# Performance work log

Hardware: AMD Instinct MI355X
Metric: run time of the kernel (lower is better)

Reference implementation:

```python
import jax, jax.numpy as jnp
import numpy as np

B, NV, NH = 256, 512, 256


def setup_inputs() -> dict:
    key = jax.random.key(0)
    k1, k2, k3, k4, k5 = jax.random.split(key, 5)
    return {
        "wt": jax.random.normal(k1, (B, NH, NV), dtype=jnp.float32),
        "varh_diag": jax.random.uniform(k2, (B, NH), dtype=jnp.float32),
        "sig2": jax.random.uniform(k3, (B,), dtype=jnp.float32),
        "b": jax.random.normal(k4, (B, NV), dtype=jnp.float32),
        "muh": jax.random.normal(k5, (B, NH), dtype=jnp.float32),
    }


def reference(wt, varh_diag, sig2, b, muh):
    # wt: [B, nh, nv], varh_diag: [B, nh], sig2: [B], b: [B, nv], muh: [B, nh]
    nv = wt.shape[2]
    w = jnp.transpose(wt, (0, 2, 1))                      # [B, nv, nh]
    # diag(varh_diag) @ wt == broadcasted row scaling (avoids materializing diag)
    varvh = varh_diag[:, :, None] * wt                    # [B, nh, nv]
    # varv = w @ varh @ wt + sig2 * I
    varv = jnp.einsum('bvh,bhu->bvu', w, varvh)           # [B, nv, nv]
    varv = varv + sig2[:, None, None] * jnp.eye(nv, dtype=wt.dtype)
    # muv = b + w @ muh
    muv = b + jnp.einsum('bvh,bh->bv', w, muh)            # [B, nv]
    mu = jnp.concatenate([muv, muh], axis=1)              # [B, nv+nh]
    # block covariance: [[varv, varvh^T], [varvh, diag(varh_diag)]]
    varh = jax.vmap(jnp.diag)(varh_diag)                  # [B, nh, nh]
    varvht = jnp.transpose(varvh, (0, 2, 1))              # [B, nv, nh]
    top = jnp.concatenate([varv, varvht], axis=2)         # [B, nv, nv+nh]
    bot = jnp.concatenate([varvh, varh], axis=2)          # [B, nh, nv+nh]
    var = jnp.concatenate([top, bot], axis=1)             # [B, nv+nh, nv+nh]
    return mu, var
```

## Files before the change

kernel.cpp:

```cpp
#include <hip/hip_runtime.h>
#include <hip/hip_bf16.h>

#define B_  256
#define NH  256
#define NV  512
#define NT  768
#define TPB 9

typedef __bf16 bf16x8 __attribute__((ext_vector_type(8)));
typedef float  f32x4  __attribute__((ext_vector_type(4)));

__device__ __forceinline__ __bf16 f2bf(float f) { return static_cast<__bf16>(f); }

__global__ __launch_bounds__(512) void fused(const float* __restrict__ wt,
                                             const float* __restrict__ varh,
                                             const float* __restrict__ sig2,
                                             const float* __restrict__ bvec,
                                             const float* __restrict__ muh,
                                             float* __restrict__ out) {
    __shared__ __align__(16) char smem[76 * 1024];

    const int bid  = blockIdx.x;
    const int q    = bid >> 3;
    const int b    = (bid & 7) * 32 + q / TPB;
    const int tile = q % TPB;
    const int t    = threadIdx.x;

    const float* wtb  = wt + (size_t)b * NH * NV;
    float* mu   = out + (size_t)b * NT;
    float* varb = out + (size_t)B_ * NT + (size_t)b * NT * NT;

    if (tile < 3) {
        const int  mt   = (tile == 1);
        const int  nt   = (tile != 0);
        const bool diag = (tile < 2);

        bf16x8 (*As)[256] = (bf16x8(*)[256])(smem);
        bf16x8 (*Bs)[256] = (bf16x8(*)[256])(smem + 32 * 1024);
        float*  varh_s    = (float*)(smem + 64 * 1024);
        float*  muh_s     = (float*)(smem + 65 * 1024);
        float (*red)[256] = (float(*)[256])(smem + 66 * 1024);

        const int m0 = mt * 256, n0 = nt * 256;
        const int lane = t & 63, wid = t >> 6;
        const int wm = wid >> 2, wn = wid & 3;
        const int mc = t & 63;
        const int kb = t >> 6;

        if (t < NH) { varh_s[t] = varh[b * NH + t]; muh_s[t] = muh[b * NH + t]; }

        f32x4 acc[8][4] = {};
        float acc_mu[4] = {0.f, 0.f, 0.f, 0.f};
        __syncthreads();

        for (int st = 0; st < 4; ++st) {
            const int k0 = st * 64;
            f32x4 av[8], bv[8];
            const float* baseA = wtb + (size_t)(k0 + kb * 8) * NV + m0 + 4 * mc;
#pragma unroll
            for (int j = 0; j < 8; ++j)
                av[j] = *reinterpret_cast<const f32x4*>(baseA + j * NV);
            if (!diag) {
                const float* baseB = wtb + (size_t)(k0 + kb * 8) * NV + n0 + 4 * mc;
#pragma unroll
                for (int j = 0; j < 8; ++j)
                    bv[j] = *reinterpret_cast<const f32x4*>(baseB + j * NV);
            }
            float sc[8];
#pragma unroll
            for (int j = 0; j < 8; ++j) sc[j] = varh_s[k0 + kb * 8 + j];

            if (diag) {
#pragma unroll
                for (int j = 0; j < 8; ++j) {
                    const float mh = muh_s[k0 + kb * 8 + j];
#pragma unroll
                    for (int mj = 0; mj < 4; ++mj) acc_mu[mj] += av[j][mj] * mh;
                }
            }

            if (st) __syncthreads();

#pragma unroll
            for (int mj = 0; mj < 4; ++mj) {
                bf16x8 pa, pb;
#pragma unroll
                for (int j = 0; j < 8; ++j) {
                    const float a  = av[j][mj];
                    const float bb = diag ? a : bv[j][mj];
                    pa[j] = f2bf(a);
                    pb[j] = f2bf(bb * sc[j]);
                }
                const int ca = 4 * mc + mj;
                const int ci = ca ^ ((ca >> 3) & 7);
                As[kb][ci] = pa;
                Bs[kb][ci] = pb;
            }
            __syncthreads();

#pragma unroll
            for (int kh = 0; kh < 2; ++kh) {
                const int ko = kh * 4 + (lane >> 4);
                bf16x8 af[8], bf4[4];
#pragma unroll
                for (int f = 0; f < 8; ++f) {
                    const int mi = wm * 128 + f * 16 + (lane & 15);
                    af[f] = As[ko][mi ^ ((mi >> 3) & 7)];
                }
#pragma unroll
                for (int f = 0; f < 4; ++f) {
                    const int ni = wn * 64 + f * 16 + (lane & 15);
                    bf4[f] = Bs[ko][ni ^ ((ni >> 3) & 7)];
                }
#pragma unroll
                for (int fm = 0; fm < 8; ++fm)
#pragma unroll
                    for (int fn = 0; fn < 4; ++fn)
                        acc[fm][fn] = __builtin_amdgcn_mfma_f32_16x16x32_bf16(
                            af[fm], bf4[fn], acc[fm][fn], 0, 0, 0);
            }
        }

        const float s2 = sig2[b];
#pragma unroll
        for (int fm = 0; fm < 8; ++fm) {
#pragma unroll
            for (int fn = 0; fn < 4; ++fn) {
                const int row = m0 + wm * 128 + fm * 16 + ((lane >> 4) << 2);
                const int col = n0 + wn * 64 + fn * 16 + (lane & 15);
#pragma unroll
                for (int r = 0; r < 4; ++r) {
                    float v = acc[fm][fn][r];
                    if (row + r == col) v += s2;
                    varb[(size_t)(row + r) * NT + col] = v;
                }
                if (!diag) {
                    *reinterpret_cast<f32x4*>(varb + (size_t)col * NT + row) =
                        acc[fm][fn];
                }
            }
        }

        if (diag) {
#pragma unroll
            for (int mj = 0; mj < 4; ++mj) red[kb][4 * mc + mj] = acc_mu[mj];
            __syncthreads();
            if (t < 256) {
                float s = 0.f;
#pragma unroll
                for (int k = 0; k < 8; ++k) s += red[k][t];
                mu[m0 + t] = bvec[b * NV + m0 + t] + s;
            }
        }
    } else if (tile < 7) {
        const int h0 = (tile - 3) * 64;
        float (*tl)[64][65] = (float(*)[64][65])smem;
        const int sub = t >> 8;
        const int tt  = t & 255;
        const int r   = tt >> 4;
        const int c4  = (tt & 15) * 4;

        for (int iter = 0; iter < 4; ++iter) {
            const int v0 = iter * 128 + sub * 64;
            if (iter) __syncthreads();
#pragma unroll
            for (int p = 0; p < 4; ++p) {
                const int h = h0 + r + 16 * p;
                const float vh = varh[b * NH + h];
                f32x4 x = *reinterpret_cast<const f32x4*>(
                    wtb + (size_t)h * NV + v0 + c4);
                x *= vh;
                *reinterpret_cast<f32x4*>(
                    varb + (size_t)(NV + h) * NT + v0 + c4) = x;
                tl[sub][r + 16 * p][c4 + 0] = x[0];
                tl[sub][r + 16 * p][c4 + 1] = x[1];
                tl[sub][r + 16 * p][c4 + 2] = x[2];
                tl[sub][r + 16 * p][c4 + 3] = x[3];
            }
            __syncthreads();
#pragma unroll
            for (int p = 0; p < 4; ++p) {
                const int vrow = v0 + r + 16 * p;
                f32x4 y;
                y[0] = tl[sub][c4 + 0][r + 16 * p];
                y[1] = tl[sub][c4 + 1][r + 16 * p];
                y[2] = tl[sub][c4 + 2][r + 16 * p];
                y[3] = tl[sub][c4 + 3][r + 16 * p];
                *reinterpret_cast<f32x4*>(
                    varb + (size_t)vrow * NT + NV + h0 + c4) = y;
            }
        }
    } else {
        const int d  = tile - 7;
        const int r0 = NV + d * 128;
        const int rr = t >> 6;
        const int c4 = (t & 63) * 4;
#pragma unroll
        for (int p = 0; p < 16; ++p) {
            const int row = rr + 8 * p;
            const int g   = d * 128 + row;
            const int dpos = g - c4;
            const float val = (dpos >= 0 && dpos < 4) ? varh[b * NH + g] : 0.f;
            f32x4 v;
            v[0] = (dpos == 0) ? val : 0.f;
            v[1] = (dpos == 1) ? val : 0.f;
            v[2] = (dpos == 2) ? val : 0.f;
            v[3] = (dpos == 3) ? val : 0.f;
            *reinterpret_cast<f32x4*>(varb + (size_t)(r0 + row) * NT + NV + c4) = v;
        }
        if (d == 0 && t < NH) mu[NV + t] = muh[b * NH + t];
    }
}

extern "C" void kernel_launch(void* const* d_in, const int* in_sizes, int n_in,
                              void* d_out, int out_size, void* d_ws, size_t ws_size,
                              hipStream_t stream) {
    (void)in_sizes; (void)n_in; (void)out_size; (void)d_ws; (void)ws_size;
    const float* wt   = (const float*)d_in[0];
    const float* varh = (const float*)d_in[1];
    const float* sig2 = (const float*)d_in[2];
    const float* bvec = (const float*)d_in[3];
    const float* muh  = (const float*)d_in[4];
    float* out = (float*)d_out;

    fused<<<B_ * TPB, 512, 0, stream>>>(wt, varh, sig2, bvec, muh, out);
}
```

Before: 161.9 us.

## Fuse varvh block writes into diagonal GEMM tiles, shrink grid to 4 tiles per batch

The four separate transpose tiles that wrote the varvh and varvh^T blocks are removed. The two diagonal GEMM tiles now write both blocks from data they already hold: the fp32 loaded wt rows scaled by varh go to the bottom-left block, and the bf16 scaled values in shared memory are converted back and written to the top-right block. This removes a second read of wt and cuts the grid from 9 to 4 blocks per batch, and the diagonal-block writer now uses nontemporal stores. The trade-off is that the top-right varvh^T block is now written from bf16-rounded values, which lowers its precision, and the diagonal tiles carry more store work, so there are fewer blocks to spread it over.

```diff
diff --git a/kernel.cpp b/kernel.cpp
--- a/kernel.cpp
+++ b/kernel.cpp
@@ -5,12 +5,16 @@
 #define NH  256
 #define NV  512
 #define NT  768
-#define TPB 9
+#define TPB 4
 
 typedef __bf16 bf16x8 __attribute__((ext_vector_type(8)));
 typedef float  f32x4  __attribute__((ext_vector_type(4)));
 
 __device__ __forceinline__ __bf16 f2bf(float f) { return static_cast<__bf16>(f); }
+
+__device__ __forceinline__ void nt_store4(float* p, f32x4 v) {
+    __builtin_nontemporal_store(v, reinterpret_cast<f32x4*>(p));
+}
 
 __global__ __launch_bounds__(512) void fused(const float* __restrict__ wt,
                                              const float* __restrict__ varh,
@@ -22,8 +26,8 @@
 
     const int bid  = blockIdx.x;
     const int q    = bid >> 3;
-    const int b    = (bid & 7) * 32 + q / TPB;
-    const int tile = q % TPB;
+    const int b    = (bid & 7) * 32 + (q >> 2);
+    const int tile = q & 3;
     const int t    = threadIdx.x;
 
     const float* wtb  = wt + (size_t)b * NH * NV;
@@ -76,6 +80,9 @@
                     const float mh = muh_s[k0 + kb * 8 + j];
 #pragma unroll
                     for (int mj = 0; mj < 4; ++mj) acc_mu[mj] += av[j][mj] * mh;
+                    f32x4 bl = av[j] * sc[j];
+                    nt_store4(varb + (size_t)(NV + k0 + kb * 8 + j) * NT + m0 + 4 * mc,
+                              bl);
                 }
             }
 
@@ -119,6 +126,23 @@
                         acc[fm][fn] = __builtin_amdgcn_mfma_f32_16x16x32_bf16(
                             af[fm], bf4[fn], acc[fm][fn], 0, 0, 0);
             }
+
+            if (diag) {
+#pragma unroll
+                for (int r = 0; r < 4; ++r) {
+                    const int vv = lane + 64 * r;
+                    const bf16x8 pv = Bs[kb][vv ^ ((vv >> 3) & 7)];
+                    f32x4 lo, hi;
+#pragma unroll
+                    for (int e = 0; e < 4; ++e) {
+                        lo[e] = (float)pv[e];
+                        hi[e] = (float)pv[e + 4];
+                    }
+                    float* dst = varb + (size_t)(m0 + vv) * NT + NV + k0 + kb * 8;
+                    *reinterpret_cast<f32x4*>(dst)     = lo;
+                    *reinterpret_cast<f32x4*>(dst + 4) = hi;
+                }
+            }
         }
 
         const float s2 = sig2[b];
@@ -128,15 +152,14 @@
             for (int fn = 0; fn < 4; ++fn) {
                 const int row = m0 + wm * 128 + fm * 16 + ((lane >> 4) << 2);
                 const int col = n0 + wn * 64 + fn * 16 + (lane & 15);
-#pragma unroll
-                for (int r = 0; r < 4; ++r) {
-                    float v = acc[fm][fn][r];
-                    if (row + r == col) v += s2;
-                    varb[(size_t)(row + r) * NT + col] = v;
-                }
+                f32x4 v = acc[fm][fn];
+                const int dpos = col - row;
+                if (dpos >= 0 && dpos < 4) v[dpos] += s2;
+#pragma unroll
+                for (int r = 0; r < 4; ++r)
+                    varb[(size_t)(row + r) * NT + col] = v[r];
                 if (!diag) {
-                    *reinterpret_cast<f32x4*>(varb + (size_t)col * NT + row) =
-                        acc[fm][fn];
+                    *reinterpret_cast<f32x4*>(varb + (size_t)col * NT + row) = v;
                 }
             }
         }
@@ -152,63 +175,18 @@
                 mu[m0 + t] = bvec[b * NV + m0 + t] + s;
             }
         }
-    } else if (tile < 7) {
-        const int h0 = (tile - 3) * 64;
-        float (*tl)[64][65] = (float(*)[64][65])smem;
-        const int sub = t >> 8;
-        const int tt  = t & 255;
-        const int r   = tt >> 4;
-        const int c4  = (tt & 15) * 4;
-
-        for (int iter = 0; iter < 4; ++iter) {
-            const int v0 = iter * 128 + sub * 64;
-            if (iter) __syncthreads();
-#pragma unroll
-            for (int p = 0; p < 4; ++p) {
-                const int h = h0 + r + 16 * p;
-                const float vh = varh[b * NH + h];
-                f32x4 x = *reinterpret_cast<const f32x4*>(
-                    wtb + (size_t)h * NV + v0 + c4);
-                x *= vh;
-                *reinterpret_cast<f32x4*>(
-                    varb + (size_t)(NV + h) * NT + v0 + c4) = x;
-                tl[sub][r + 16 * p][c4 + 0] = x[0];
-                tl[sub][r + 16 * p][c4 + 1] = x[1];
-                tl[sub][r + 16 * p][c4 + 2] = x[2];
-                tl[sub][r + 16 * p][c4 + 3] = x[3];
-            }
-            __syncthreads();
-#pragma unroll
-            for (int p = 0; p < 4; ++p) {
-                const int vrow = v0 + r + 16 * p;
-                f32x4 y;
-                y[0] = tl[sub][c4 + 0][r + 16 * p];
-                y[1] = tl[sub][c4 + 1][r + 16 * p];
-                y[2] = tl[sub][c4 + 2][r + 16 * p];
-                y[3] = tl[sub][c4 + 3][r + 16 * p];
-                *reinterpret_cast<f32x4*>(
-                    varb + (size_t)vrow * NT + NV + h0 + c4) = y;
-            }
-        }
     } else {
-        const int d  = tile - 7;
-        const int r0 = NV + d * 128;
         const int rr = t >> 6;
         const int c4 = (t & 63) * 4;
 #pragma unroll
-        for (int p = 0; p < 16; ++p) {
+        for (int p = 0; p < 32; ++p) {
             const int row = rr + 8 * p;
-            const int g   = d * 128 + row;
-            const int dpos = g - c4;
-            const float val = (dpos >= 0 && dpos < 4) ? varh[b * NH + g] : 0.f;
-            f32x4 v;
-            v[0] = (dpos == 0) ? val : 0.f;
-            v[1] = (dpos == 1) ? val : 0.f;
-            v[2] = (dpos == 2) ? val : 0.f;
-            v[3] = (dpos == 3) ? val : 0.f;
-            *reinterpret_cast<f32x4*>(varb + (size_t)(r0 + row) * NT + NV + c4) = v;
-        }
-        if (d == 0 && t < NH) mu[NV + t] = muh[b * NH + t];
+            const int dpos = row - c4;
+            f32x4 v = {0.f, 0.f, 0.f, 0.f};
+            if (dpos >= 0 && dpos < 4) v[dpos] = varh[b * NH + row];
+            nt_store4(varb + (size_t)(NV + row) * NT + NV + c4, v);
+        }
+        if (t < NH) mu[NV + t] = muh[b * NH + t];
     }
 }
 
```

Result: slower. 190.2 us (+17.5%).
